# Kernel optimization log

Measured on AMD Instinct MI355X. Metric: run time of the kernel, lower is better.

The kernel has to match this reference:

```python
import jax, jax.numpy as jnp
import numpy as np

NUM_Y_STEPS = 10
NUM_TYPES = 3
ANCHOR_DIM = 3 * NUM_Y_STEPS + 1  # 31
EPS = 1e-9


def setup_inputs() -> dict:
    key = jax.random.key(0)
    k1, k2, k3, k4, k5, k6 = jax.random.split(key, 6)
    B, A = 8192, 26
    D = NUM_TYPES * ANCHOR_DIM  # 93
    pred = jax.random.uniform(k1, (B, A, D), dtype=jnp.float32)
    gt = jax.random.uniform(k2, (B, A, D), dtype=jnp.float32)
    pred_hcam = jax.random.uniform(k3, (B,), dtype=jnp.float32) + 1.0
    gt_hcam = jax.random.uniform(k4, (B,), dtype=jnp.float32) + 1.0
    pred_pitch = jax.random.normal(k5, (B,), dtype=jnp.float32)
    gt_pitch = jax.random.normal(k6, (B,), dtype=jnp.float32)
    return {
        'pred_3D_lanes': pred,
        'gt_3D_lanes': gt,
        'pred_hcam': pred_hcam,
        'gt_hcam': gt_hcam,
        'pred_pitch': pred_pitch,
        'gt_pitch': gt_pitch,
    }


def reference(pred_3D_lanes, gt_3D_lanes, pred_hcam, gt_hcam, pred_pitch, gt_pitch):
    B, A, _ = pred_3D_lanes.shape
    K = NUM_Y_STEPS
    pred = pred_3D_lanes.reshape(B, A, NUM_TYPES, ANCHOR_DIM)
    gt = gt_3D_lanes.reshape(B, A, NUM_TYPES, ANCHOR_DIM)

    pred_class = pred[..., -1:]                # [B,A,T,1]
    pred_anchors = pred[..., : 2 * K]          # [B,A,T,2K]
    pred_vis = pred[..., 2 * K : 3 * K]        # [B,A,T,K]
    gt_class = gt[..., -1:]
    gt_anchors = gt[..., : 2 * K]
    gt_vis = gt[..., 2 * K : 3 * K]

    # loss0: binary cross entropy on visibility (note: (1-gt+eps) as in original)
    loss0 = -jnp.sum(
        gt_vis * jnp.log(pred_vis + EPS)
        + (1.0 - gt_vis + EPS) * jnp.log(1.0 - pred_vis + EPS)
    ) / K

    # loss1: binary cross entropy on lane class probability
    loss1 = -jnp.sum(
        gt_class * jnp.log(pred_class + EPS)
        + (1.0 - gt_class) * jnp.log(1.0 - pred_class + EPS)
    )

    # loss2: visibility/class-masked L1 on X-offset and Z anchors
    vis2 = jnp.concatenate([gt_vis, gt_vis], axis=3)  # [B,A,T,2K]
    loss2 = jnp.sum(jnp.abs(gt_class * vis2 * (pred_anchors - gt_anchors)))

    total = loss0 + loss1 + loss2
    return (total, loss0, loss1, loss2)
```

## Files before the change

kernel.cpp:

```cpp
#include <hip/hip_runtime.h>

#define EPSL 1e-9f
#define NGROUPS 638976
#define NBLOCKS (NGROUPS / 256)
#define NSLOTS 64

typedef float v4u __attribute__((ext_vector_type(4), aligned(4)));

__global__ __launch_bounds__(256) void laneline_reduce_kernel(
    const float* __restrict__ pred,
    const float* __restrict__ gt,
    float* __restrict__ ws)
{
    const int g = blockIdx.x * 256 + threadIdx.x;
    const float* p = pred + (size_t)g * 31;
    const float* q = gt   + (size_t)g * 31;

    v4u pa[5], qa[5];
#pragma unroll
    for (int c = 0; c < 5; ++c) {
        pa[c] = *(const v4u*)(p + 4 * c);
        qa[c] = *(const v4u*)(q + 4 * c);
    }
    const v4u pv0 = *(const v4u*)(p + 20), pv1 = *(const v4u*)(p + 24);
    const v4u qv0 = *(const v4u*)(q + 20), qv1 = *(const v4u*)(q + 24);
    const float pv8 = p[28], pv9 = p[29], pcl = p[30];
    const float qv8 = q[28], qv9 = q[29], qcl = q[30];

    const float pvis[10] = {pv0[0], pv0[1], pv0[2], pv0[3],
                            pv1[0], pv1[1], pv1[2], pv1[3], pv8, pv9};
    const float gvis[10] = {qv0[0], qv0[1], qv0[2], qv0[3],
                            qv1[0], qv1[1], qv1[2], qv1[3], qv8, qv9};
    float pan[20], qan[20];
#pragma unroll
    for (int c = 0; c < 5; ++c)
#pragma unroll
        for (int k = 0; k < 4; ++k) {
            pan[4 * c + k] = pa[c][k];
            qan[4 * c + k] = qa[c][k];
        }

    float s0 = 0.f, s2 = 0.f;
#pragma unroll
    for (int i = 0; i < 10; ++i) {
        const float gv = gvis[i];
        s2 += qcl * gv * (fabsf(pan[i]      - qan[i])
                        + fabsf(pan[10 + i] - qan[10 + i]));
        const float pv = pvis[i];
        s0 += gv * __logf(pv + EPSL)
            + (1.0f - gv + EPSL) * __logf(1.0f - pv + EPSL);
    }
    float s1 = qcl * __logf(pcl + EPSL)
             + (1.0f - qcl) * __logf(1.0f - pcl + EPSL);

#pragma unroll
    for (int off = 32; off > 0; off >>= 1) {
        s0 += __shfl_down(s0, off, 64);
        s1 += __shfl_down(s1, off, 64);
        s2 += __shfl_down(s2, off, 64);
    }
    const int lane = threadIdx.x & 63;
    const int wid  = threadIdx.x >> 6;
    if (lane == 0) {
        float* slot = ws + ((((unsigned)blockIdx.x << 2) + wid) & (NSLOTS - 1)) * 16;
        atomicAdd(&slot[0], s0);
        atomicAdd(&slot[1], s1);
        atomicAdd(&slot[2], s2);
    }
}

__global__ __launch_bounds__(64) void laneline_finalize_kernel(
    const float* __restrict__ ws, float* __restrict__ out)
{
    const int t = threadIdx.x;
    float v0 = ws[t * 16], v1 = ws[t * 16 + 1], v2 = ws[t * 16 + 2];
#pragma unroll
    for (int off = 32; off > 0; off >>= 1) {
        v0 += __shfl_down(v0, off, 64);
        v1 += __shfl_down(v1, off, 64);
        v2 += __shfl_down(v2, off, 64);
    }
    if (t == 0) {
        const float l0 = -v0 * 0.1f;
        const float l1 = -v1;
        const float l2 =  v2;
        out[0] = l0 + l1 + l2;
        out[1] = l0;
        out[2] = l1;
        out[3] = l2;
    }
}

extern "C" void kernel_launch(void* const* d_in, const int* in_sizes, int n_in,
                              void* d_out, int out_size, void* d_ws, size_t ws_size,
                              hipStream_t stream)
{
    const float* pred = (const float*)d_in[0];
    const float* gt   = (const float*)d_in[1];
    float* ws  = (float*)d_ws;
    float* out = (float*)d_out;

    hipMemsetAsync(ws, 0, NSLOTS * 16 * sizeof(float), stream);

    laneline_reduce_kernel<<<NBLOCKS, 256, 0, stream>>>(pred, gt, ws);
    laneline_finalize_kernel<<<1, 64, 0, stream>>>(ws, out);
}
```

Before: 187.7 us.

## Remap reduction to 32-lane-per-row coalesced loads with persistent grid-stride blocks

Each 31-float anchor group is now read by 32 lanes, one element per lane, so global loads coalesce instead of each thread issuing strided unaligned vector loads. Visibility and class values are fetched from neighbouring lanes with ds_bpermute, and masks pick which loss term each lane adds to. The grid is cut to a fixed number of blocks that walk the rows with a 4-way unrolled grid-stride loop. Blocks combine their wave partials in shared memory so only one thread per block issues the atomics. In exchange every lane computes two logs whether or not it needs them, and the bpermutes add LDS traffic.

```diff
diff --git a/kernel.cpp b/kernel.cpp
--- a/kernel.cpp
+++ b/kernel.cpp
@@ -2,70 +2,74 @@
 
 #define EPSL 1e-9f
 #define NGROUPS 638976
-#define NBLOCKS (NGROUPS / 256)
+#define NB 2496
+#define ROWS_PER_BLOCK 8
+#define RSTRIDE (NB * ROWS_PER_BLOCK)
+#define NSTEPS (NGROUPS / RSTRIDE)
+#define UNROLL 4
 #define NSLOTS 64
-
-typedef float v4u __attribute__((ext_vector_type(4), aligned(4)));
 
 __global__ __launch_bounds__(256) void laneline_reduce_kernel(
     const float* __restrict__ pred,
     const float* __restrict__ gt,
     float* __restrict__ ws)
 {
-    const int g = blockIdx.x * 256 + threadIdx.x;
-    const float* p = pred + (size_t)g * 31;
-    const float* q = gt   + (size_t)g * 31;
+    const int tid  = threadIdx.x;
+    const int lane = tid & 63;
+    const int d    = tid & 31;
+    const int dc   = (d < 31) ? d : 30;
 
-    v4u pa[5], qa[5];
+    const int rowbase = lane & 32;
+    const int idxVis  = (rowbase + 20 + (d % 10)) * 4;
+    const int idxCls  = (rowbase + 30) * 4;
+    const float mA = (d < 20) ? 1.f : 0.f;
+    const float mV = (d >= 20 && d < 30) ? 1.f : 0.f;
+    const float mC = (d == 30) ? 1.f : 0.f;
+
+    const int row0 = blockIdx.x * ROWS_PER_BLOCK + (tid >> 5);
+    size_t base = (size_t)row0 * 31 + dc;
+    const size_t stride = (size_t)RSTRIDE * 31;
+
+    float a0 = 0.f, a1 = 0.f, a2 = 0.f;
+#pragma unroll 1
+    for (int s = 0; s < NSTEPS; s += UNROLL) {
+        float pv[UNROLL], gv[UNROLL];
 #pragma unroll
-    for (int c = 0; c < 5; ++c) {
-        pa[c] = *(const v4u*)(p + 4 * c);
-        qa[c] = *(const v4u*)(q + 4 * c);
+        for (int u = 0; u < UNROLL; ++u) {
+            pv[u] = pred[base + (size_t)u * stride];
+            gv[u] = gt[base + (size_t)u * stride];
+        }
+#pragma unroll
+        for (int u = 0; u < UNROLL; ++u) {
+            const float p = pv[u], g = gv[u];
+            const float gvis = __int_as_float(
+                __builtin_amdgcn_ds_bpermute(idxVis, __float_as_int(g)));
+            const float gcls = __int_as_float(
+                __builtin_amdgcn_ds_bpermute(idxCls, __float_as_int(g)));
+            const float lp1 = __logf(p + EPSL);
+            const float lp2 = __logf(1.0f - p + EPSL);
+            a2 = fmaf(mA, gcls * gvis * fabsf(p - g), a2);
+            a0 = fmaf(mV, fmaf(g, lp1, (1.0f - g + EPSL) * lp2), a0);
+            a1 = fmaf(mC, fmaf(g, lp1, (1.0f - g) * lp2), a1);
+        }
+        base += (size_t)UNROLL * stride;
     }
-    const v4u pv0 = *(const v4u*)(p + 20), pv1 = *(const v4u*)(p + 24);
-    const v4u qv0 = *(const v4u*)(q + 20), qv1 = *(const v4u*)(q + 24);
-    const float pv8 = p[28], pv9 = p[29], pcl = p[30];
-    const float qv8 = q[28], qv9 = q[29], qcl = q[30];
-
-    const float pvis[10] = {pv0[0], pv0[1], pv0[2], pv0[3],
-                            pv1[0], pv1[1], pv1[2], pv1[3], pv8, pv9};
-    const float gvis[10] = {qv0[0], qv0[1], qv0[2], qv0[3],
-                            qv1[0], qv1[1], qv1[2], qv1[3], qv8, qv9};
-    float pan[20], qan[20];
-#pragma unroll
-    for (int c = 0; c < 5; ++c)
-#pragma unroll
-        for (int k = 0; k < 4; ++k) {
-            pan[4 * c + k] = pa[c][k];
-            qan[4 * c + k] = qa[c][k];
-        }
-
-    float s0 = 0.f, s2 = 0.f;
-#pragma unroll
-    for (int i = 0; i < 10; ++i) {
-        const float gv = gvis[i];
-        s2 += qcl * gv * (fabsf(pan[i]      - qan[i])
-                        + fabsf(pan[10 + i] - qan[10 + i]));
-        const float pv = pvis[i];
-        s0 += gv * __logf(pv + EPSL)
-            + (1.0f - gv + EPSL) * __logf(1.0f - pv + EPSL);
-    }
-    float s1 = qcl * __logf(pcl + EPSL)
-             + (1.0f - qcl) * __logf(1.0f - pcl + EPSL);
 
 #pragma unroll
     for (int off = 32; off > 0; off >>= 1) {
-        s0 += __shfl_down(s0, off, 64);
-        s1 += __shfl_down(s1, off, 64);
-        s2 += __shfl_down(s2, off, 64);
+        a0 += __shfl_down(a0, off, 64);
+        a1 += __shfl_down(a1, off, 64);
+        a2 += __shfl_down(a2, off, 64);
     }
-    const int lane = threadIdx.x & 63;
-    const int wid  = threadIdx.x >> 6;
-    if (lane == 0) {
-        float* slot = ws + ((((unsigned)blockIdx.x << 2) + wid) & (NSLOTS - 1)) * 16;
-        atomicAdd(&slot[0], s0);
-        atomicAdd(&slot[1], s1);
-        atomicAdd(&slot[2], s2);
+    __shared__ float red[12];
+    const int wid = tid >> 6;
+    if (lane == 0) { red[wid] = a0; red[4 + wid] = a1; red[8 + wid] = a2; }
+    __syncthreads();
+    if (tid == 0) {
+        float* slot = ws + (blockIdx.x & (NSLOTS - 1)) * 16;
+        atomicAdd(&slot[0], red[0] + red[1] + red[2]  + red[3]);
+        atomicAdd(&slot[1], red[4] + red[5] + red[6]  + red[7]);
+        atomicAdd(&slot[2], red[8] + red[9] + red[10] + red[11]);
     }
 }
 
@@ -102,6 +106,6 @@
 
     hipMemsetAsync(ws, 0, NSLOTS * 16 * sizeof(float), stream);
 
-    laneline_reduce_kernel<<<NBLOCKS, 256, 0, stream>>>(pred, gt, ws);
+    laneline_reduce_kernel<<<NB, 256, 0, stream>>>(pred, gt, ws);
     laneline_finalize_kernel<<<1, 64, 0, stream>>>(ws, out);
 }
```

New measurement: 191.1 us. No clear change (+1.8%).
